# Kernel tuning notes

Hardware: AMD Instinct MI355X
Metric: run time of the kernel (lower is better)

Reference implementation:

```python
import jax, jax.numpy as jnp
import numpy as np

D = 1024  # bilinear_dim
IN_A = 1024
IN_B = 1024

def setup_inputs() -> dict:
    key = jax.random.key(0)
    ks = jax.random.split(key, 8)
    B, La, Lb = 64, 256, 256
    sa = 1.0 / np.sqrt(IN_A)
    sb = 1.0 / np.sqrt(IN_B)
    sd = 1.0 / np.sqrt(D)
    return {
        "a": jax.random.normal(ks[0], (B, La, IN_A), dtype=jnp.float32),
        "b": jax.random.normal(ks[1], (B, Lb, IN_B), dtype=jnp.float32),
        "Wa": jax.random.uniform(ks[2], (IN_A, D), jnp.float32, -sa, sa),
        "ba": jax.random.uniform(ks[3], (D,), jnp.float32, -sa, sa),
        "Wb": jax.random.uniform(ks[4], (IN_B, D), jnp.float32, -sb, sb),
        "bb": jax.random.uniform(ks[5], (D,), jnp.float32, -sb, sb),
        "w": jax.random.uniform(ks[6], (D,), jnp.float32, -sd, sd),
        "wbias": jax.random.uniform(ks[7], (), jnp.float32, -sd, sd),
    }

def reference(a, b, Wa, ba, Wb, bb, w, wbias):
    # Linear projections (dropout inactive at inference)
    pa = a @ Wa + ba          # (B, La, D)
    pb = b @ Wb + bb          # (B, Lb, D)
    # Fused bilinear score: sum_d w[d]*pa[b,i,d]*pb[b,j,d] + wbias
    # (equivalent to materializing (B,La,Lb,D) outer product then Linear(D->1))
    scores = jnp.einsum('bid,bjd->bij', pa * w, pb) + wbias  # (B, La, Lb)
    B, La, Lb = scores.shape
    norm = jax.nn.softmax(scores.reshape(B, La * Lb), axis=1)
    return norm.reshape(B, La, Lb)
```

## Files before the change

kernel.cpp:

```cpp
#include <hip/hip_runtime.h>
#include <hip/hip_bf16.h>

typedef __attribute__((ext_vector_type(8))) short bf16x8;
typedef __attribute__((ext_vector_type(4))) float f32x4;

#define K_DIM 1024
#define M_PROJ 16384
#define NBATCH 64
#define SEQ 256

static __device__ inline unsigned short bf16_bits(float f) {
    __hip_bfloat16 h = __float2bfloat16(f);
    return *reinterpret_cast<unsigned short*>(&h);
}

#define GLOAD16(g, l) __builtin_amdgcn_global_load_lds(                          \
    (__attribute__((address_space(1))) void*)(g),                                \
    (__attribute__((address_space(3))) void*)(l), 16, 0, 0)

__global__ __launch_bounds__(256) void uvc_kernel(const float* __restrict__ Wa,
                                                  const float* __restrict__ Wb,
                                                  const float* __restrict__ w,
                                                  const float* __restrict__ ba,
                                                  const float* __restrict__ bb,
                                                  float* __restrict__ u,
                                                  float* __restrict__ v,
                                                  float* __restrict__ c)
{
    __shared__ float psum[4];
    const int p = blockIdx.x;
    const int t = threadIdx.x;
    const int d0 = t * 4;

    float part = 0.f;
    if (p < 1024) {
        float4 m = *(const float4*)&Wa[(size_t)p * K_DIM + d0];
        float4 ww = *(const float4*)&w[d0];
        float4 bv = *(const float4*)&bb[d0];
        part = m.x * ww.x * bv.x + m.y * ww.y * bv.y + m.z * ww.z * bv.z + m.w * ww.w * bv.w;
    } else if (p < 2048) {
        float4 m = *(const float4*)&Wb[(size_t)(p - 1024) * K_DIM + d0];
        float4 ww = *(const float4*)&w[d0];
        float4 bv = *(const float4*)&ba[d0];
        part = m.x * ww.x * bv.x + m.y * ww.y * bv.y + m.z * ww.z * bv.z + m.w * ww.w * bv.w;
    } else {
        float4 ww = *(const float4*)&w[d0];
        float4 b1 = *(const float4*)&ba[d0];
        float4 b2 = *(const float4*)&bb[d0];
        part = ww.x * b1.x * b2.x + ww.y * b1.y * b2.y + ww.z * b1.z * b2.z + ww.w * b1.w * b2.w;
    }
#pragma unroll
    for (int off = 32; off; off >>= 1) part += __shfl_down(part, off);
    if ((t & 63) == 0) psum[t >> 6] = part;
    __syncthreads();
    if (t == 0) {
        const float s = (psum[0] + psum[1]) + (psum[2] + psum[3]);
        if (p < 1024) u[p] = s;
        else if (p < 2048) v[p - 1024] = s;
        else *c = s;
    }
}

__global__ __launch_bounds__(256) void wscale_conv(const float* __restrict__ in,
                                                   const float* __restrict__ w,
                                                   unsigned short* __restrict__ out,
                                                   int scale_by_w)
{
    const int i = blockIdx.x * 256 + threadIdx.x;
    const int d0 = (i * 8) & (K_DIM - 1);
    const float4* p = reinterpret_cast<const float4*>(in) + (size_t)i * 2;
    float4 v0 = p[0], v1 = p[1];
    if (scale_by_w) {
        float4 w0 = *(const float4*)&w[d0];
        float4 w1 = *(const float4*)&w[d0 + 4];
        v0.x *= w0.x; v0.y *= w0.y; v0.z *= w0.z; v0.w *= w0.w;
        v1.x *= w1.x; v1.y *= w1.y; v1.z *= w1.z; v1.w *= w1.w;
    }
    unsigned short uo[8];
    uo[0] = bf16_bits(v0.x); uo[1] = bf16_bits(v0.y); uo[2] = bf16_bits(v0.z); uo[3] = bf16_bits(v0.w);
    uo[4] = bf16_bits(v1.x); uo[5] = bf16_bits(v1.y); uo[6] = bf16_bits(v1.z); uo[7] = bf16_bits(v1.w);
    *reinterpret_cast<uint4*>(out + (size_t)i * 8) = *reinterpret_cast<uint4*>(uo);
}

__global__ __launch_bounds__(256) void conv_rows(const float* __restrict__ X,
                                                 const float* __restrict__ dvec,
                                                 unsigned short* __restrict__ out,
                                                 float* __restrict__ rowdot)
{
    __shared__ float psum[4];
    const int t = threadIdx.x;
    const int r = blockIdx.x * 2 + (t >> 7);
    const int c8 = (t & 127) * 8;

    const float* xp = &X[(size_t)r * K_DIM + c8];
    float4 v0 = *(const float4*)xp;
    float4 v1 = *(const float4*)(xp + 4);
    float4 u0 = *(const float4*)&dvec[c8];
    float4 u1 = *(const float4*)&dvec[c8 + 4];
    float part = v0.x * u0.x + v0.y * u0.y + v0.z * u0.z + v0.w * u0.w
               + v1.x * u1.x + v1.y * u1.y + v1.z * u1.z + v1.w * u1.w;

    unsigned short uo[8];
    uo[0] = bf16_bits(v0.x); uo[1] = bf16_bits(v0.y); uo[2] = bf16_bits(v0.z); uo[3] = bf16_bits(v0.w);
    uo[4] = bf16_bits(v1.x); uo[5] = bf16_bits(v1.y); uo[6] = bf16_bits(v1.z); uo[7] = bf16_bits(v1.w);
    *reinterpret_cast<uint4*>(&out[(size_t)r * K_DIM + c8]) = *reinterpret_cast<uint4*>(uo);

#pragma unroll
    for (int off = 32; off; off >>= 1) part += __shfl_down(part, off);
    if ((t & 63) == 0) psum[t >> 6] = part;
    __syncthreads();
    if ((t & 127) == 0) rowdot[r] = psum[(t >> 6)] + psum[(t >> 6) + 1];
}

__global__ __launch_bounds__(256) void mt_gemm(const __hip_bfloat16* __restrict__ Wb16,
                                               const __hip_bfloat16* __restrict__ Waw,
                                               unsigned short* __restrict__ Mt)
{
    __shared__ __align__(16) unsigned short As[128][32];
    __shared__ __align__(16) unsigned short Bs[128][32];

    const int tid  = threadIdx.x;
    const int lane = tid & 63;
    const int wave = tid >> 6;
    const int q0 = blockIdx.x * 128;
    const int p0 = blockIdx.y * 128;
    const int wr = (wave >> 1) * 64;
    const int wc = (wave & 1) * 64;

    const __hip_bfloat16* Arow = Wb16 + (size_t)q0 * K_DIM;
    const __hip_bfloat16* Brow = Waw + (size_t)p0 * K_DIM;

    f32x4 acc[4][4];
#pragma unroll
    for (int i = 0; i < 4; ++i)
#pragma unroll
        for (int j = 0; j < 4; ++j) acc[i][j] = f32x4{0.f, 0.f, 0.f, 0.f};

    const int lrow = lane & 15;
    const int kq   = (lane >> 4) * 8;

    for (int k0 = 0; k0 < K_DIM; k0 += 32) {
        __syncthreads();
#pragma unroll
        for (int it = 0; it < 2; ++it) {
            const int chunk = (it * 4 + wave) * 64 + lane;
            const int row = chunk >> 2;
            const int col = (chunk & 3) * 8;
            GLOAD16(Arow + (size_t)row * K_DIM + k0 + col,
                    reinterpret_cast<char*>(&As[0][0]) + (it * 4 + wave) * 1024);
        }
#pragma unroll
        for (int it = 0; it < 2; ++it) {
            const int chunk = (it * 4 + wave) * 64 + lane;
            const int row = chunk >> 2;
            const int col = (chunk & 3) * 8;
            GLOAD16(Brow + (size_t)row * K_DIM + k0 + col,
                    reinterpret_cast<char*>(&Bs[0][0]) + (it * 4 + wave) * 1024);
        }
        __syncthreads();

        bf16x8 af[4], bfr[4];
#pragma unroll
        for (int f = 0; f < 4; ++f) {
            af[f]  = *reinterpret_cast<const bf16x8*>(&As[wr + f * 16 + lrow][kq]);
            bfr[f] = *reinterpret_cast<const bf16x8*>(&Bs[wc + f * 16 + lrow][kq]);
        }
#pragma unroll
        for (int i = 0; i < 4; ++i)
#pragma unroll
            for (int j = 0; j < 4; ++j)
                acc[i][j] = __builtin_amdgcn_mfma_f32_16x16x32_bf16(bfr[j], af[i], acc[i][j], 0, 0, 0);
    }

#pragma unroll
    for (int ii = 0; ii < 4; ++ii) {
        const int q = q0 + wr + ii * 16 + lrow;
#pragma unroll
        for (int jj = 0; jj < 4; ++jj) {
            const int pb = p0 + wc + jj * 16 + (lane >> 4) * 4;
            unsigned short uo[4];
            uo[0] = bf16_bits(acc[ii][jj][0]);
            uo[1] = bf16_bits(acc[ii][jj][1]);
            uo[2] = bf16_bits(acc[ii][jj][2]);
            uo[3] = bf16_bits(acc[ii][jj][3]);
            *(ushort4*)&Mt[(size_t)q * K_DIM + pb] = *(ushort4*)uo;
        }
    }
}

__global__ __launch_bounds__(512, 2) void proj_gemm256(
    const __hip_bfloat16* __restrict__ A,
    const __hip_bfloat16* __restrict__ Wt,
    const float* __restrict__ bias,
    const float* __restrict__ scale,
    __hip_bfloat16* __restrict__ out,
    int use_bias, int use_scale)
{
    __shared__ __align__(16) unsigned short lds[2][4][128 * 64];

    const int tid  = threadIdx.x;
    const int lane = tid & 63;
    const int w    = tid >> 6;
    const int wr   = w >> 2;
    const int wc   = w & 3;
    const int m0 = blockIdx.x * 256;
    const int n0 = blockIdx.y * 256;

    const int c1 = w * 128 + lane, c2 = c1 + 64;
    const int r1 = c1 >> 3, r2 = c2 >> 3;
    const int k1 = (c1 & 7) ^ (r1 & 7);
    const int k2 = (c2 & 7) ^ (r2 & 7);

    const int lrow = lane & 15;
    const int kq0  = (((lane >> 4) + 0) ^ (lane & 7)) * 16;
    const int kq1  = (((lane >> 4) + 4) ^ (lane & 7)) * 16;

#define STG(SRC, RB, KB, BUF, REG)                                               \
    {                                                                            \
        GLOAD16((SRC) + (size_t)((RB) + r1) * K_DIM + (KB) + k1 * 8,             \
                (char*)(&lds[BUF][REG][0]) + w * 2048);                          \
        GLOAD16((SRC) + (size_t)((RB) + r2) * K_DIM + (KB) + k2 * 8,             \
                (char*)(&lds[BUF][REG][0]) + w * 2048 + 1024);                   \
    }

    f32x4 acc[8][4];
#pragma unroll
    for (int i = 0; i < 8; ++i)
#pragma unroll
        for (int j = 0; j < 4; ++j) acc[i][j] = f32x4{0.f, 0.f, 0.f, 0.f};

    STG(A,  m0,       0, 0, 0); STG(A,  m0 + 128,  0, 0, 1);
    STG(Wt, n0,       0, 0, 2); STG(Wt, n0 + 128,  0, 0, 3);
    STG(A,  m0,      64, 1, 0); STG(A,  m0 + 128, 64, 1, 1);
    asm volatile("s_waitcnt vmcnt(4)" ::: "memory");
    __builtin_amdgcn_sched_barrier(0);
    __builtin_amdgcn_s_barrier();

#define KTILE(CUR, NXT, T)                                                       \
    {                                                                            \
        const int kb1 = (((T) + 1) & 15) << 6;                                   \
        const int kb2 = (((T) + 2) & 15) << 6;                                   \
        const char* Ab = (const char*)(&lds[CUR][wr][0]);                        \
        const char* Bb = (const char*)(&lds[CUR][2 + (wc >> 1)][0])              \
                         + (wc & 1) * 8192;                                      \
        bf16x8 af[4][2], bfr[4][2];                                              \
        _Pragma("unroll")                                                        \
        for (int mi = 0; mi < 4; ++mi) {                                         \
            af[mi][0] = *(const bf16x8*)(Ab + mi * 2048 + lrow * 128 + kq0);     \
            af[mi][1] = *(const bf16x8*)(Ab + mi * 2048 + lrow * 128 + kq1);     \
        }                                                                        \
        _Pragma("unroll")                                                        \
        for (int nj = 0; nj < 2; ++nj) {                                         \
            bfr[nj][0] = *(const bf16x8*)(Bb + nj * 2048 + lrow * 128 + kq0);    \
            bfr[nj][1] = *(const bf16x8*)(Bb + nj * 2048 + lrow * 128 + kq1);    \
        }                                                                        \
        STG(Wt, n0, kb1, NXT, 2);                                                \
        __builtin_amdgcn_sched_barrier(0);                                       \
        __builtin_amdgcn_s_barrier();                                            \
        asm volatile("s_waitcnt lgkmcnt(0)" ::: "memory");                       \
        __builtin_amdgcn_sched_barrier(0);                                       \
        __builtin_amdgcn_s_setprio(1);                                           \
        _Pragma("unroll")                                                        \
        for (int mi = 0; mi < 4; ++mi)                                           \
            _Pragma("unroll")                                                    \
            for (int nj = 0; nj < 2; ++nj) {                                     \
                acc[mi][nj] = __builtin_amdgcn_mfma_f32_16x16x32_bf16(           \
                    af[mi][0], bfr[nj][0], acc[mi][nj], 0, 0, 0);                \
                acc[mi][nj] = __builtin_amdgcn_mfma_f32_16x16x32_bf16(           \
                    af[mi][1], bfr[nj][1], acc[mi][nj], 0, 0, 0);                \
            }                                                                    \
        __builtin_amdgcn_s_setprio(0);                                           \
        __builtin_amdgcn_sched_barrier(0);                                       \
        __builtin_amdgcn_s_barrier();                                            \
        _Pragma("unroll")                                                        \
        for (int nj = 2; nj < 4; ++nj) {                                         \
            bfr[nj][0] = *(const bf16x8*)(Bb + nj * 2048 + lrow * 128 + kq0);    \
            bfr[nj][1] = *(const bf16x8*)(Bb + nj * 2048 + lrow * 128 + kq1);    \
        }                                                                        \
        STG(Wt, n0 + 128, kb1, NXT, 3);                                          \
        __builtin_amdgcn_sched_barrier(0);                                       \
        __builtin_amdgcn_s_barrier();                                            \
        asm volatile("s_waitcnt lgkmcnt(0)" ::: "memory");                       \
        __builtin_amdgcn_sched_barrier(0);                                       \
        __builtin_amdgcn_s_setprio(1);                                           \
        _Pragma("unroll")                                                        \
        for (int mi = 0; mi < 4; ++mi)                                           \
            _Pragma("unroll")                                                    \
            for (int nj = 2; nj < 4; ++nj) {                                     \
                acc[mi][nj] = __builtin_amdgcn_mfma_f32_16x16x32_bf16(           \
                    af[mi][0], bfr[nj][0], acc[mi][nj], 0, 0, 0);                \
                acc[mi][nj] = __builtin_amdgcn_mfma_f32_16x16x32_bf16(           \
                    af[mi][1], bfr[nj][1], acc[mi][nj], 0, 0, 0);                \
            }                                                                    \
        __builtin_amdgcn_s_setprio(0);                                           \
        __builtin_amdgcn_sched_barrier(0);                                       \
        __builtin_amdgcn_s_barrier();                                            \
        _Pragma("unroll")                                                        \
        for (int mi = 0; mi < 4; ++mi) {                                         \
            af[mi][0] = *(const bf16x8*)(Ab + 8192 + mi * 2048 + lrow * 128 + kq0);\
            af[mi][1] = *(const bf16x8*)(Ab + 8192 + mi * 2048 + lrow * 128 + kq1);\
        }                                                                        \
        __builtin_amdgcn_sched_barrier(0);                                       \
        __builtin_amdgcn_s_barrier();                                            \
        asm volatile("s_waitcnt lgkmcnt(0)" ::: "memory");                       \
        __builtin_amdgcn_sched_barrier(0);                                       \
        __builtin_amdgcn_s_setprio(1);                                           \
        _Pragma("unroll")                                                        \
        for (int mi = 0; mi < 4; ++mi)                                           \
            _Pragma("unroll")                                                    \
            for (int nj = 0; nj < 2; ++nj) {                                     \
                acc[4 + mi][nj] = __builtin_amdgcn_mfma_f32_16x16x32_bf16(       \
                    af[mi][0], bfr[nj][0], acc[4 + mi][nj], 0, 0, 0);            \
                acc[4 + mi][nj] = __builtin_amdgcn_mfma_f32_16x16x32_bf16(       \
                    af[mi][1], bfr[nj][1], acc[4 + mi][nj], 0, 0, 0);            \
            }                                                                    \
        __builtin_amdgcn_s_setprio(0);                                           \
        __builtin_amdgcn_sched_barrier(0);                                       \
        __builtin_amdgcn_s_barrier();                                            \
        STG(A, m0,       kb2, CUR, 0);                                           \
        STG(A, m0 + 128, kb2, CUR, 1);                                           \
        __builtin_amdgcn_sched_barrier(0);                                       \
        __builtin_amdgcn_s_barrier();                                            \
        __builtin_amdgcn_s_setprio(1);                                           \
        _Pragma("unroll")                                                        \
        for (int mi = 0; mi < 4; ++mi)                                           \
            _Pragma("unroll")                                                    \
            for (int nj = 2; nj < 4; ++nj) {                                     \
                acc[4 + mi][nj] = __builtin_amdgcn_mfma_f32_16x16x32_bf16(       \
                    af[mi][0], bfr[nj][0], acc[4 + mi][nj], 0, 0, 0);            \
                acc[4 + mi][nj] = __builtin_amdgcn_mfma_f32_16x16x32_bf16(       \
                    af[mi][1], bfr[nj][1], acc[4 + mi][nj], 0, 0, 0);            \
            }                                                                    \
        __builtin_amdgcn_s_setprio(0);                                           \
        asm volatile("s_waitcnt vmcnt(4)" ::: "memory");                         \
        __builtin_amdgcn_sched_barrier(0);                                       \
        __builtin_amdgcn_s_barrier();                                            \
    }

    for (int tt = 0; tt < 8; ++tt) {
        const int t0 = tt * 2;
        KTILE(0, 1, t0);
        KTILE(1, 0, t0 + 1);
    }
    asm volatile("s_waitcnt vmcnt(0)" ::: "memory");
#undef KTILE
#undef STG

#pragma unroll
    for (int nj = 0; nj < 4; ++nj) {
        const int col = n0 + wc * 64 + nj * 16 + lrow;
        const float bc = use_bias ? bias[col] : 0.0f;
        const float sc = use_scale ? scale[col] : 1.0f;
#pragma unroll
        for (int mi8 = 0; mi8 < 8; ++mi8) {
            const int rowoff = (mi8 >> 2) * 64 + (mi8 & 3) * 16;
#pragma unroll
            for (int r = 0; r < 4; ++r) {
                const int row = m0 + wr * 128 + rowoff + (lane >> 4) * 4 + r;
                out[(size_t)row * K_DIM + col] = __float2bfloat16((acc[mi8][nj][r] + bc) * sc);
            }
        }
    }
}

__global__ __launch_bounds__(256) void score_gemm(const __hip_bfloat16* __restrict__ T,
                                                  const __hip_bfloat16* __restrict__ Bbf,
                                                  const float* __restrict__ alpha,
                                                  const float* __restrict__ beta,
                                                  const float* __restrict__ cptr,
                                                  const float* __restrict__ wbias,
                                                  float* __restrict__ out,
                                                  float* __restrict__ partials)
{
    __shared__ __align__(16) unsigned short As[128][32];
    __shared__ __align__(16) unsigned short Bs[128][32];
    __shared__ float psum[4];

    const int tid  = threadIdx.x;
    const int lane = tid & 63;
    const int wave = tid >> 6;
    const int b  = blockIdx.z;
    const int i0 = blockIdx.x * 128;
    const int j0 = blockIdx.y * 128;
    const int wr = (wave >> 1) * 64;
    const int wc = (wave & 1) * 64;

    const __hip_bfloat16* Arow = T + (size_t)(b * SEQ + i0) * K_DIM;
    const __hip_bfloat16* Brow = Bbf + (size_t)(b * SEQ + j0) * K_DIM;

    f32x4 acc[4][4];
#pragma unroll
    for (int i = 0; i < 4; ++i)
#pragma unroll
        for (int j = 0; j < 4; ++j) acc[i][j] = f32x4{0.f, 0.f, 0.f, 0.f};

    const int lrow = lane & 15;
    const int kq   = (lane >> 4) * 8;

    for (int k0 = 0; k0 < K_DIM; k0 += 32) {
        __syncthreads();
#pragma unroll
        for (int it = 0; it < 2; ++it) {
            const int chunk = (it * 4 + wave) * 64 + lane;
            const int row = chunk >> 2;
            const int col = (chunk & 3) * 8;
            GLOAD16(Arow + (size_t)row * K_DIM + k0 + col,
                    reinterpret_cast<char*>(&As[0][0]) + (it * 4 + wave) * 1024);
        }
#pragma unroll
        for (int it = 0; it < 2; ++it) {
            const int chunk = (it * 4 + wave) * 64 + lane;
            const int row = chunk >> 2;
            const int col = (chunk & 3) * 8;
            GLOAD16(Brow + (size_t)row * K_DIM + k0 + col,
                    reinterpret_cast<char*>(&Bs[0][0]) + (it * 4 + wave) * 1024);
        }
        __syncthreads();

        bf16x8 af[4], bfr[4];
#pragma unroll
        for (int f = 0; f < 4; ++f) {
            af[f]  = *reinterpret_cast<const bf16x8*>(&As[wr + f * 16 + lrow][kq]);
            bfr[f] = *reinterpret_cast<const bf16x8*>(&Bs[wc + f * 16 + lrow][kq]);
        }
#pragma unroll
        for (int i = 0; i < 4; ++i)
#pragma unroll
            for (int j = 0; j < 4; ++j)
                acc[i][j] = __builtin_amdgcn_mfma_f32_16x16x32_bf16(bfr[j], af[i], acc[i][j], 0, 0, 0);
    }

    const float cwb = *cptr + *wbias;
    float lsum = 0.f;
#pragma unroll
    for (int ii = 0; ii < 4; ++ii) {
        const int i = i0 + wr + ii * 16 + lrow;
        const float av = alpha[b * SEQ + i] + cwb;
#pragma unroll
        for (int jj = 0; jj < 4; ++jj) {
            const int jb = j0 + wc + jj * 16 + (lane >> 4) * 4;
            const float4 bv = *(const float4*)&beta[b * SEQ + jb];
            float4 e;
            e.x = __expf(acc[ii][jj][0] + av + bv.x);
            e.y = __expf(acc[ii][jj][1] + av + bv.y);
            e.z = __expf(acc[ii][jj][2] + av + bv.z);
            e.w = __expf(acc[ii][jj][3] + av + bv.w);
            lsum += (e.x + e.y) + (e.z + e.w);
            *(float4*)&out[(size_t)b * (SEQ * SEQ) + (size_t)i * SEQ + jb] = e;
        }
    }
#pragma unroll
    for (int off = 32; off; off >>= 1) lsum += __shfl_down(lsum, off);
    if (lane == 0) psum[wave] = lsum;
    __syncthreads();
    if (tid == 0)
        partials[b * 4 + blockIdx.x * 2 + blockIdx.y] =
            (psum[0] + psum[1]) + (psum[2] + psum[3]);
}

__global__ __launch_bounds__(1024) void normalize_k(float* __restrict__ s,
                                                    const float* __restrict__ partials)
{
    const int b    = blockIdx.x >> 2;
    const int part = blockIdx.x & 3;
    const float inv = 1.0f / (((partials[b * 4 + 0] + partials[b * 4 + 1]) +
                               partials[b * 4 + 2]) + partials[b * 4 + 3]);
    float4* p4 = reinterpret_cast<float4*>(s + (size_t)b * (SEQ * SEQ));
    const int base = part * 4096;
#pragma unroll
    for (int it = 0; it < 4; ++it) {
        const int i = base + it * 1024 + threadIdx.x;
        float4 v = p4[i];
        v.x *= inv; v.y *= inv; v.z *= inv; v.w *= inv;
        p4[i] = v;
    }
}

extern "C" void kernel_launch(void* const* d_in, const int* in_sizes, int n_in,
                              void* d_out, int out_size, void* d_ws, size_t ws_size,
                              hipStream_t stream)
{
    const float* a     = (const float*)d_in[0];
    const float* b     = (const float*)d_in[1];
    const float* Wa    = (const float*)d_in[2];
    const float* ba    = (const float*)d_in[3];
    const float* Wb    = (const float*)d_in[4];
    const float* bb    = (const float*)d_in[5];
    const float* w     = (const float*)d_in[6];
    const float* wbias = (const float*)d_in[7];
    float* out = (float*)d_out;

    char* wsb = (char*)d_ws;
    unsigned short* Waw   = (unsigned short*)(wsb);
    unsigned short* Wb16  = (unsigned short*)(wsb + (size_t)2097152);
    unsigned short* Mt    = (unsigned short*)(wsb + (size_t)4194304);
    float* u              = (float*)(wsb + (size_t)6291456);
    float* v              = (float*)(wsb + (size_t)6291456 + 4096);
    float* c              = (float*)(wsb + (size_t)6291456 + 8192);
    float* alpha          = (float*)(wsb + (size_t)6291456 + 16384);
    float* beta           = (float*)(wsb + (size_t)6291456 + 16384 + 65536);
    float* partials       = (float*)(wsb + (size_t)6291456 + 16384 + 131072);
    unsigned short* ab16  = (unsigned short*)(wsb + (size_t)8388608);
    unsigned short* Tbuf  = (unsigned short*)(wsb + (size_t)41943040);

    uvc_kernel<<<2049, 256, 0, stream>>>(Wa, Wb, w, ba, bb, u, v, c);
    wscale_conv<<<512, 256, 0, stream>>>(Wa, w, Waw, 1);
    wscale_conv<<<512, 256, 0, stream>>>(Wb, w, Wb16, 0);
    mt_gemm<<<dim3(8, 8), 256, 0, stream>>>((const __hip_bfloat16*)Wb16,
                                            (const __hip_bfloat16*)Waw, Mt);
    conv_rows<<<M_PROJ / 2, 256, 0, stream>>>(a, u, ab16, alpha);
    const dim3 pgrid(M_PROJ / 256, K_DIM / 256);
    proj_gemm256<<<pgrid, 512, 0, stream>>>((const __hip_bfloat16*)ab16,
                                            (const __hip_bfloat16*)Mt,
                                            u, u, (__hip_bfloat16*)Tbuf, 0, 0);
    conv_rows<<<M_PROJ / 2, 256, 0, stream>>>(b, v, ab16, beta);
    const dim3 sgrid(SEQ / 128, SEQ / 128, NBATCH);
    score_gemm<<<sgrid, 256, 0, stream>>>((const __hip_bfloat16*)Tbuf,
                                          (const __hip_bfloat16*)ab16,
                                          alpha, beta, c, wbias, out, partials);
    normalize_k<<<NBATCH * 4, 1024, 0, stream>>>(out, partials);
}
```

Measured before the change: 138.3 us.

## Merge weight prep kernels and stage projection GEMM epilogue through LDS

Merges the three small weight-preparation launches (u/v/c reductions and two bf16 conversions) into one kernel, which removes launch overhead. In the 256x256 projection GEMM it swaps the MFMA operand order so each lane holds four consecutive output columns. The epilogue then writes bf16 results into XOR-swizzled shared memory and stores them to global as coalesced 16-byte rows, replacing scattered 2-byte stores. This adds an extra barrier and reuses the operand LDS buffer, which assumes that buffer is large enough for the 256x256 bf16 tile.

```diff
diff --git a/kernel.cpp b/kernel.cpp
--- a/kernel.cpp
+++ b/kernel.cpp
@@ -18,20 +18,42 @@
     (__attribute__((address_space(1))) void*)(g),                                \
     (__attribute__((address_space(3))) void*)(l), 16, 0, 0)
 
-__global__ __launch_bounds__(256) void uvc_kernel(const float* __restrict__ Wa,
-                                                  const float* __restrict__ Wb,
-                                                  const float* __restrict__ w,
-                                                  const float* __restrict__ ba,
-                                                  const float* __restrict__ bb,
-                                                  float* __restrict__ u,
-                                                  float* __restrict__ v,
-                                                  float* __restrict__ c)
-{
+__global__ __launch_bounds__(256) void prep(const float* __restrict__ Wa,
+                                            const float* __restrict__ Wb,
+                                            const float* __restrict__ w,
+                                            const float* __restrict__ ba,
+                                            const float* __restrict__ bb,
+                                            unsigned short* __restrict__ Waw,
+                                            unsigned short* __restrict__ Wb16,
+                                            float* __restrict__ u,
+                                            float* __restrict__ v,
+                                            float* __restrict__ c)
+{
+    const int blk = blockIdx.x;
+    const int t = threadIdx.x;
+    if (blk < 1024) {
+        const int scale_by_w = (blk < 512);
+        const float* in = scale_by_w ? Wa : Wb;
+        unsigned short* out = scale_by_w ? Waw : Wb16;
+        const int i = (scale_by_w ? blk : blk - 512) * 256 + t;
+        const int d0 = (i * 8) & (K_DIM - 1);
+        const float4* p = reinterpret_cast<const float4*>(in) + (size_t)i * 2;
+        float4 v0 = p[0], v1 = p[1];
+        if (scale_by_w) {
+            float4 w0 = *(const float4*)&w[d0];
+            float4 w1 = *(const float4*)&w[d0 + 4];
+            v0.x *= w0.x; v0.y *= w0.y; v0.z *= w0.z; v0.w *= w0.w;
+            v1.x *= w1.x; v1.y *= w1.y; v1.z *= w1.z; v1.w *= w1.w;
+        }
+        unsigned short uo[8];
+        uo[0] = bf16_bits(v0.x); uo[1] = bf16_bits(v0.y); uo[2] = bf16_bits(v0.z); uo[3] = bf16_bits(v0.w);
+        uo[4] = bf16_bits(v1.x); uo[5] = bf16_bits(v1.y); uo[6] = bf16_bits(v1.z); uo[7] = bf16_bits(v1.w);
+        *reinterpret_cast<uint4*>(out + (size_t)i * 8) = *reinterpret_cast<uint4*>(uo);
+        return;
+    }
     __shared__ float psum[4];
-    const int p = blockIdx.x;
-    const int t = threadIdx.x;
+    const int p = blk - 1024;
     const int d0 = t * 4;
-
     float part = 0.f;
     if (p < 1024) {
         float4 m = *(const float4*)&Wa[(size_t)p * K_DIM + d0];
@@ -61,27 +83,6 @@
     }
 }
 
-__global__ __launch_bounds__(256) void wscale_conv(const float* __restrict__ in,
-                                                   const float* __restrict__ w,
-                                                   unsigned short* __restrict__ out,
-                                                   int scale_by_w)
-{
-    const int i = blockIdx.x * 256 + threadIdx.x;
-    const int d0 = (i * 8) & (K_DIM - 1);
-    const float4* p = reinterpret_cast<const float4*>(in) + (size_t)i * 2;
-    float4 v0 = p[0], v1 = p[1];
-    if (scale_by_w) {
-        float4 w0 = *(const float4*)&w[d0];
-        float4 w1 = *(const float4*)&w[d0 + 4];
-        v0.x *= w0.x; v0.y *= w0.y; v0.z *= w0.z; v0.w *= w0.w;
-        v1.x *= w1.x; v1.y *= w1.y; v1.z *= w1.z; v1.w *= w1.w;
-    }
-    unsigned short uo[8];
-    uo[0] = bf16_bits(v0.x); uo[1] = bf16_bits(v0.y); uo[2] = bf16_bits(v0.z); uo[3] = bf16_bits(v0.w);
-    uo[4] = bf16_bits(v1.x); uo[5] = bf16_bits(v1.y); uo[6] = bf16_bits(v1.z); uo[7] = bf16_bits(v1.w);
-    *reinterpret_cast<uint4*>(out + (size_t)i * 8) = *reinterpret_cast<uint4*>(uo);
-}
-
 __global__ __launch_bounds__(256) void conv_rows(const float* __restrict__ X,
                                                  const float* __restrict__ dvec,
                                                  unsigned short* __restrict__ out,
@@ -265,9 +266,9 @@
             _Pragma("unroll")                                                    \
             for (int nj = 0; nj < 2; ++nj) {                                     \
                 acc[mi][nj] = __builtin_amdgcn_mfma_f32_16x16x32_bf16(           \
-                    af[mi][0], bfr[nj][0], acc[mi][nj], 0, 0, 0);                \
+                    bfr[nj][0], af[mi][0], acc[mi][nj], 0, 0, 0);                \
                 acc[mi][nj] = __builtin_amdgcn_mfma_f32_16x16x32_bf16(           \
-                    af[mi][1], bfr[nj][1], acc[mi][nj], 0, 0, 0);                \
+                    bfr[nj][1], af[mi][1], acc[mi][nj], 0, 0, 0);                \
             }                                                                    \
         __builtin_amdgcn_s_setprio(0);                                           \
         __builtin_amdgcn_sched_barrier(0);                                       \
@@ -288,9 +289,9 @@
             _Pragma("unroll")                                                    \
             for (int nj = 2; nj < 4; ++nj) {                                     \
                 acc[mi][nj] = __builtin_amdgcn_mfma_f32_16x16x32_bf16(           \
-                    af[mi][0], bfr[nj][0], acc[mi][nj], 0, 0, 0);                \
+                    bfr[nj][0], af[mi][0], acc[mi][nj], 0, 0, 0);                \
                 acc[mi][nj] = __builtin_amdgcn_mfma_f32_16x16x32_bf16(           \
-                    af[mi][1], bfr[nj][1], acc[mi][nj], 0, 0, 0);                \
+                    bfr[nj][1], af[mi][1], acc[mi][nj], 0, 0, 0);                \
             }                                                                    \
         __builtin_amdgcn_s_setprio(0);                                           \
         __builtin_amdgcn_sched_barrier(0);                                       \
@@ -310,9 +311,9 @@
             _Pragma("unroll")                                                    \
             for (int nj = 0; nj < 2; ++nj) {                                     \
                 acc[4 + mi][nj] = __builtin_amdgcn_mfma_f32_16x16x32_bf16(       \
-                    af[mi][0], bfr[nj][0], acc[4 + mi][nj], 0, 0, 0);            \
+                    bfr[nj][0], af[mi][0], acc[4 + mi][nj], 0, 0, 0);            \
                 acc[4 + mi][nj] = __builtin_amdgcn_mfma_f32_16x16x32_bf16(       \
-                    af[mi][1], bfr[nj][1], acc[4 + mi][nj], 0, 0, 0);            \
+                    bfr[nj][1], af[mi][1], acc[4 + mi][nj], 0, 0, 0);            \
             }                                                                    \
         __builtin_amdgcn_s_setprio(0);                                           \
         __builtin_amdgcn_sched_barrier(0);                                       \
@@ -327,9 +328,9 @@
             _Pragma("unroll")                                                    \
             for (int nj = 2; nj < 4; ++nj) {                                     \
                 acc[4 + mi][nj] = __builtin_amdgcn_mfma_f32_16x16x32_bf16(       \
-                    af[mi][0], bfr[nj][0], acc[4 + mi][nj], 0, 0, 0);            \
+                    bfr[nj][0], af[mi][0], acc[4 + mi][nj], 0, 0, 0);            \
                 acc[4 + mi][nj] = __builtin_amdgcn_mfma_f32_16x16x32_bf16(       \
-                    af[mi][1], bfr[nj][1], acc[4 + mi][nj], 0, 0, 0);            \
+                    bfr[nj][1], af[mi][1], acc[4 + mi][nj], 0, 0, 0);            \
             }                                                                    \
         __builtin_amdgcn_s_setprio(0);                                           \
         asm volatile("s_waitcnt vmcnt(4)" ::: "memory");                         \
@@ -342,23 +343,43 @@
         KTILE(0, 1, t0);
         KTILE(1, 0, t0 + 1);
     }
-    asm volatile("s_waitcnt vmcnt(0)" ::: "memory");
 #undef KTILE
 #undef STG
 
-#pragma unroll
-    for (int nj = 0; nj < 4; ++nj) {
-        const int col = n0 + wc * 64 + nj * 16 + lrow;
-        const float bc = use_bias ? bias[col] : 0.0f;
-        const float sc = use_scale ? scale[col] : 1.0f;
-#pragma unroll
-        for (int mi8 = 0; mi8 < 8; ++mi8) {
-            const int rowoff = (mi8 >> 2) * 64 + (mi8 & 3) * 16;
-#pragma unroll
-            for (int r = 0; r < 4; ++r) {
-                const int row = m0 + wr * 128 + rowoff + (lane >> 4) * 4 + r;
-                out[(size_t)row * K_DIM + col] = __float2bfloat16((acc[mi8][nj][r] + bc) * sc);
-            }
+    asm volatile("s_waitcnt vmcnt(0)" ::: "memory");
+    __builtin_amdgcn_sched_barrier(0);
+    __builtin_amdgcn_s_barrier();
+    char* eb = (char*)(&lds[0][0][0]);
+#pragma unroll
+    for (int mi8 = 0; mi8 < 8; ++mi8) {
+        const int ml = wr * 128 + (mi8 >> 2) * 64 + (mi8 & 3) * 16 + lrow;
+#pragma unroll
+        for (int nj = 0; nj < 4; ++nj) {
+            const int nl = wc * 64 + nj * 16 + (lane >> 4) * 4;
+            const int nb = n0 + nl;
+            float4 bc = float4{0.f, 0.f, 0.f, 0.f};
+            float4 sc = float4{1.f, 1.f, 1.f, 1.f};
+            if (use_bias)  bc = *(const float4*)&bias[nb];
+            if (use_scale) sc = *(const float4*)&scale[nb];
+            unsigned short uo[4];
+            uo[0] = bf16_bits((acc[mi8][nj][0] + bc.x) * sc.x);
+            uo[1] = bf16_bits((acc[mi8][nj][1] + bc.y) * sc.y);
+            uo[2] = bf16_bits((acc[mi8][nj][2] + bc.z) * sc.z);
+            uo[3] = bf16_bits((acc[mi8][nj][3] + bc.w) * sc.w);
+            const int v = nl >> 3;
+            *(ushort4*)(eb + ml * 512 + ((v ^ (ml & 7)) * 16) + ((nl >> 2) & 1) * 8)
+                = *(ushort4*)uo;
+        }
+    }
+    __syncthreads();
+#pragma unroll
+    for (int p = 0; p < 2; ++p) {
+        const int ml = p * 128 + (tid >> 2);
+#pragma unroll
+        for (int it = 0; it < 8; ++it) {
+            const int v = it * 4 + (tid & 3);
+            uint4 val = *(const uint4*)(eb + ml * 512 + ((v ^ (ml & 7)) * 16));
+            *(uint4*)&out[(size_t)(m0 + ml) * K_DIM + n0 + v * 8] = val;
         }
     }
 }
@@ -503,9 +524,7 @@
     unsigned short* ab16  = (unsigned short*)(wsb + (size_t)8388608);
     unsigned short* Tbuf  = (unsigned short*)(wsb + (size_t)41943040);
 
-    uvc_kernel<<<2049, 256, 0, stream>>>(Wa, Wb, w, ba, bb, u, v, c);
-    wscale_conv<<<512, 256, 0, stream>>>(Wa, w, Waw, 1);
-    wscale_conv<<<512, 256, 0, stream>>>(Wb, w, Wb16, 0);
+    prep<<<3073, 256, 0, stream>>>(Wa, Wb, w, ba, bb, Waw, Wb16, u, v, c);
     mt_gemm<<<dim3(8, 8), 256, 0, stream>>>((const __hip_bfloat16*)Wb16,
                                             (const __hip_bfloat16*)Waw, Mt);
     conv_rows<<<M_PROJ / 2, 256, 0, stream>>>(a, u, ab16, alpha);
```

New measurement: 128.9 us. -6.8%, faster.
